# Optimization experiments

Hardware: AMD Instinct MI355X
Metric: run time of the kernel (lower is better)

The kernel has to match this reference:

```python
import jax, jax.numpy as jnp
import numpy as np

HEADS = 12
DIM_HEAD = 64

def setup_inputs() -> dict:
    key = jax.random.key(0)
    ks = jax.random.split(key, 5)
    B, S, D = 4, 2048, 768
    s = 0.02
    return {
        "x": jax.random.normal(ks[0], (B, S, D), dtype=jnp.float32),
        "Wq": jax.random.normal(ks[1], (D, D), dtype=jnp.float32) * s,
        "Wk": jax.random.normal(ks[2], (D, D), dtype=jnp.float32) * s,
        "Wv": jax.random.normal(ks[3], (D, D), dtype=jnp.float32) * s,
        "Wo": jax.random.normal(ks[4], (D, D), dtype=jnp.float32) * s,
        "bo": jnp.zeros((D,), dtype=jnp.float32),
    }

def reference(x, Wq, Wk, Wv, Wo, bo):
    B, S, D = x.shape
    H, Dh = HEADS, DIM_HEAD
    scale = Dh ** -0.5
    # projections (torch Linear: x @ W^T)
    q = (x @ Wq.T).reshape(B, S, H, Dh).transpose(0, 2, 1, 3) * scale  # [B,H,S,Dh]
    k = (x @ Wk.T).reshape(B, S, H, Dh).transpose(0, 2, 1, 3)
    v = (x @ Wv.T).reshape(B, S, H, Dh).transpose(0, 2, 1, 3)
    sim = jnp.einsum("bhid,bhjd->bhij", q, k)  # [B,H,S,S]
    mask_value = -jnp.finfo(sim.dtype).max
    causal_mask = jnp.triu(jnp.ones((S, S), dtype=bool), k=1)
    sim = jnp.where(causal_mask, mask_value, sim)
    attn = jax.nn.softmax(sim, axis=-1)
    # dropout is identity in eval mode
    out = jnp.einsum("bhij,bhjd->bhid", attn, v)  # [B,H,S,Dh]
    out = out.transpose(0, 2, 1, 3).reshape(B, S, H * Dh)
    return out @ Wo.T + bo
```

## Files before the change

kernel.cpp:

```cpp
#include <hip/hip_runtime.h>
#include <stdint.h>

typedef unsigned short u16;
typedef __bf16 bf16x8 __attribute__((ext_vector_type(8)));
typedef float f32x4 __attribute__((ext_vector_type(4)));
typedef u16 u16x4 __attribute__((ext_vector_type(4)));
typedef u16 u16x8 __attribute__((ext_vector_type(8)));
typedef uint32_t u32x2 __attribute__((ext_vector_type(2)));

#define LDS_CAST(p) (reinterpret_cast<__attribute__((address_space(3))) uint32_t*>(reinterpret_cast<uintptr_t>(p)))
#define GLB_CAST(p) (reinterpret_cast<const __attribute__((address_space(1))) uint32_t*>(reinterpret_cast<uintptr_t>(p)))
#define GLOAD16(g, l) __builtin_amdgcn_global_load_lds(GLB_CAST(g), LDS_CAST(l), 16, 0, 0)
#define AS3U16(p) (reinterpret_cast<__attribute__((address_space(3))) u16*>(reinterpret_cast<uintptr_t>(p)))

__device__ __forceinline__ u16 f2bf(float f) {
    uint32_t u = __builtin_bit_cast(uint32_t, f);
    u += 0x7fffu + ((u >> 16) & 1u);
    return (u16)(u >> 16);
}
__device__ __forceinline__ u16 bfbits(float f) {
    return __builtin_bit_cast(u16, (__bf16)f);
}

__global__ void cast_all(const float* __restrict__ x,
                         const float* __restrict__ a, const float* __restrict__ b,
                         const float* __restrict__ c, const float* __restrict__ d,
                         u16* __restrict__ ox, u16* __restrict__ oa, u16* __restrict__ ob,
                         u16* __restrict__ oc, u16* __restrict__ od) {
    const int bid = blockIdx.x;
    const float* in;
    u16* out;
    int i;
    if (bid < 6144) {
        in = x; out = ox; i = bid * 256 + threadIdx.x;
    } else {
        const int zb = bid - 6144;
        const int z = zb / 576, lb = zb % 576;
        in = (z == 0) ? a : (z == 1) ? b : (z == 2) ? c : d;
        out = (z == 0) ? oa : (z == 1) ? ob : (z == 2) ? oc : od;
        i = lb * 256 + threadIdx.x;
    }
    float4 f = reinterpret_cast<const float4*>(in)[i];
    u16x4 o;
    o.x = f2bf(f.x); o.y = f2bf(f.y); o.z = f2bf(f.z); o.w = f2bf(f.w);
    reinterpret_cast<u16x4*>(out)[i] = o;
}

__global__ __launch_bounds__(256) void gemm_qkv(
    const u16* __restrict__ X, const u16* __restrict__ Wq,
    const u16* __restrict__ Wk, const u16* __restrict__ Wv,
    u16* __restrict__ qo, u16* __restrict__ ko, u16* __restrict__ vTo)
{
    __shared__ u16 As[2][128 * 32];
    __shared__ u16 Bs[2][128 * 32];
    const int tid = threadIdx.x;
    const int lane = tid & 63;
    const int w = tid >> 6;
    const int lr = lane & 15, lg = lane >> 4;
    const int wrow = (w >> 1) * 64, wcol = (w & 1) * 64;

    const int lin = blockIdx.x + blockIdx.y * 6 + blockIdx.z * 384;
    const int xcd = lin & 7, idx = lin >> 3;
    const int prow = xcd * 8 + idx / 18;
    const int rem = idx % 18;
    const int bxc = rem % 6, z = rem / 6;
    const int row0 = prow * 128, col0 = bxc * 128;
    const u16* Wt = (z == 0) ? Wq : (z == 1) ? Wk : Wv;

    f32x4 acc[4][4];
#pragma unroll
    for (int m = 0; m < 4; ++m)
#pragma unroll
        for (int n = 0; n < 4; ++n)
#pragma unroll
            for (int j = 0; j < 4; ++j) acc[m][n][j] = 0.f;

#define QSTAGE(KT)                                                                                 \
    {                                                                                              \
        const int buf_ = (KT) & 1;                                                                 \
        _Pragma("unroll")                                                                          \
        for (int it = 0; it < 2; ++it) {                                                           \
            const int c = it * 256 + w * 64 + lane;                                                \
            const int row = c >> 2, c16 = c & 3;                                                   \
            GLOAD16(X  + (size_t)(row0 + row) * 768 + (KT) * 32 + c16 * 8, &As[buf_][(it * 256 + w * 64) * 8]); \
            GLOAD16(Wt + (size_t)(col0 + row) * 768 + (KT) * 32 + c16 * 8, &Bs[buf_][(it * 256 + w * 64) * 8]); \
        }                                                                                          \
    }

#define QSTEP(KT, VN, PF)                                                                          \
    {                                                                                              \
        if (PF) QSTAGE((KT) + 1);                                                                  \
        asm volatile("s_waitcnt vmcnt(" #VN ")" ::: "memory");                                     \
        __builtin_amdgcn_s_barrier();                                                              \
        const int cur_ = (KT) & 1;                                                                 \
        bf16x8 af[4], bfr[4];                                                                      \
        _Pragma("unroll")                                                                          \
        for (int m = 0; m < 4; ++m) af[m] = *(const bf16x8*)&As[cur_][(wrow + m * 16 + lr) * 32 + lg * 8]; \
        _Pragma("unroll")                                                                          \
        for (int n = 0; n < 4; ++n) bfr[n] = *(const bf16x8*)&Bs[cur_][(wcol + n * 16 + lr) * 32 + lg * 8]; \
        asm volatile("s_waitcnt lgkmcnt(0)" ::: "memory");                                         \
        __builtin_amdgcn_sched_barrier(0);                                                         \
        __builtin_amdgcn_s_barrier();                                                              \
        _Pragma("unroll")                                                                          \
        for (int m = 0; m < 4; ++m)                                                                \
            _Pragma("unroll")                                                                      \
            for (int n = 0; n < 4; ++n)                                                            \
                acc[m][n] = __builtin_amdgcn_mfma_f32_16x16x32_bf16(af[m], bfr[n], acc[m][n], 0, 0, 0); \
    }

    QSTAGE(0);
    for (int kt = 0; kt < 23; ++kt) QSTEP(kt, 4, true);
    QSTEP(23, 0, false);
#undef QSTEP
#undef QSTAGE

    if (z == 2) {
#pragma unroll
        for (int n = 0; n < 4; ++n) {
            const int j = col0 + wcol + n * 16 + lr;
            const int h = j >> 6, dh = j & 63;
#pragma unroll
            for (int m = 0; m < 4; ++m) {
                const int i0 = row0 + wrow + m * 16 + lg * 4;
                const int b = i0 >> 11, s0 = i0 & 2047;
                u16x4 pk;
#pragma unroll
                for (int r = 0; r < 4; ++r) pk[r] = bfbits(acc[m][n][r]);
                *(u16x4*)&vTo[(((size_t)b * 12 + h) * 64 + dh) * 2048 + s0] = pk;
            }
        }
    } else {
        u16* outp = (z == 0) ? qo : ko;
        const float scl = (z == 0) ? 0.18033688011112042f : 1.0f;
#pragma unroll
        for (int n = 0; n < 4; ++n) {
            const int j = col0 + wcol + n * 16 + lr;
            const int h = j >> 6, dh = j & 63;
#pragma unroll
            for (int m = 0; m < 4; ++m)
#pragma unroll
                for (int r = 0; r < 4; ++r) {
                    const int i = row0 + wrow + m * 16 + lg * 4 + r;
                    const int b = i >> 11, s = i & 2047;
                    outp[(((size_t)b * 12 + h) * 2048 + s) * 64 + dh] = bfbits(acc[m][n][r] * scl);
                }
        }
    }
}

template<bool DIAG>
__device__ __forceinline__ void attn_step(
    const bf16x8* aq, f32x4* o, float* lrow,
    const u16* __restrict__ Ksb, const u16* __restrict__ Vsb, u16* __restrict__ PT,
    int kvb, int qg0, int lr, int lg)
{
    f32x4 sacc[4];
#pragma unroll
    for (int n = 0; n < 4; ++n)
#pragma unroll
        for (int j = 0; j < 4; ++j) sacc[n][j] = 0.f;
    __builtin_amdgcn_s_setprio(1);
#pragma unroll
    for (int kk = 0; kk < 2; ++kk)
#pragma unroll
        for (int n = 0; n < 4; ++n) {
            const int row = n * 16 + lr;
            const int p = (kk * 4 + lg) ^ (row & 7);
            bf16x8 bk = *(const bf16x8*)&Ksb[row * 64 + p * 8];
            sacc[n] = __builtin_amdgcn_mfma_f32_16x16x32_bf16(aq[kk], bk, sacc[n], 0, 0, 0);
        }
    __builtin_amdgcn_s_setprio(0);

    float pv[4][4];
#pragma unroll
    for (int r = 0; r < 4; ++r) {
        float ls = 0.f;
#pragma unroll
        for (int n = 0; n < 4; ++n) {
            float sv = sacc[n][r];
            if (DIAG && (kvb + n * 16 + lr) > qg0 + r) sv = -1e30f;
            const float e = __builtin_amdgcn_exp2f(sv);
            pv[r][n] = e;
            ls += e;
        }
        lrow[r] += ls;
    }

#pragma unroll
    for (int n = 0; n < 4; ++n) {
        u16x4 pk;
#pragma unroll
        for (int r = 0; r < 4; ++r) pk[r] = bfbits(pv[r][n]);
        *(u16x4*)&PT[(n * 16 + lr) * 16 + lg * 4] = pk;
    }

    u32x2 t0, t1, t2, t3;
    __attribute__((address_space(3))) u16* pb = AS3U16(PT) + lg * 128 + lr * 4;
    asm volatile("ds_read_b64_tr_b16 %0, %1" : "=v"(t0) : "v"(pb) : "memory");
    asm volatile("ds_read_b64_tr_b16 %0, %1 offset:128" : "=v"(t1) : "v"(pb) : "memory");
    asm volatile("ds_read_b64_tr_b16 %0, %1 offset:1024" : "=v"(t2) : "v"(pb) : "memory");
    asm volatile("ds_read_b64_tr_b16 %0, %1 offset:1152" : "=v"(t3) : "v"(pb) : "memory");
    asm volatile("s_waitcnt lgkmcnt(0)" ::: "memory");
    __builtin_amdgcn_sched_barrier(0);
    union { u32x2 h[2]; bf16x8 v; } ua, ub;
    ua.h[0] = t0; ua.h[1] = t1;
    ub.h[0] = t2; ub.h[1] = t3;
    const bf16x8 ap0 = ua.v, ap1 = ub.v;

    __builtin_amdgcn_s_setprio(1);
#pragma unroll
    for (int n = 0; n < 4; ++n) {
        const int rowv = n * 16 + lr;
        const int p0 = (0 + lg) ^ (rowv & 7);
        const int p1 = (4 + lg) ^ (rowv & 7);
        bf16x8 bv0 = *(const bf16x8*)&Vsb[rowv * 64 + p0 * 8];
        bf16x8 bv1 = *(const bf16x8*)&Vsb[rowv * 64 + p1 * 8];
        o[n] = __builtin_amdgcn_mfma_f32_16x16x32_bf16(ap0, bv0, o[n], 0, 0, 0);
        o[n] = __builtin_amdgcn_mfma_f32_16x16x32_bf16(ap1, bv1, o[n], 0, 0, 0);
    }
    __builtin_amdgcn_s_setprio(0);
}

__global__ __launch_bounds__(256) void attn_kernel(
    const u16* __restrict__ q, const u16* __restrict__ k,
    const u16* __restrict__ vT, u16* __restrict__ attn)
{
    __shared__ u16 Ks[2][64 * 64];
    __shared__ u16 Vs[2][64 * 64];
    __shared__ u16 Ps[4][64 * 16];

    const int lin = blockIdx.x + (blockIdx.y << 4);
    const int logi = (lin & 7) * 96 + (lin >> 3);
    const int pair = logi & 15, bh = logi >> 4;

    const int qA = pair, qB = 31 - pair;
    const int tid = threadIdx.x, lane = tid & 63, w = tid >> 6;
    const int lr = lane & 15, lg = lane >> 4;

    const u16* Kp = k + (size_t)bh * 2048 * 64;
    const u16* Vp = vT + (size_t)bh * 64 * 2048;

    const u16* QpA = q + ((size_t)bh * 2048 + qA * 64 + w * 16) * 64;
    const u16* QpB = q + ((size_t)bh * 2048 + qB * 64 + w * 16) * 64;
    bf16x8 aqA[2], aqB[2];
    aqA[0] = *(const bf16x8*)&QpA[lr * 64 + lg * 8];
    aqA[1] = *(const bf16x8*)&QpA[lr * 64 + 32 + lg * 8];
    aqB[0] = *(const bf16x8*)&QpB[lr * 64 + lg * 8];
    aqB[1] = *(const bf16x8*)&QpB[lr * 64 + 32 + lg * 8];

    f32x4 oA[4], oB[4];
    float lA[4], lB[4];
#pragma unroll
    for (int n = 0; n < 4; ++n)
#pragma unroll
        for (int j = 0; j < 4; ++j) { oA[n][j] = 0.f; oB[n][j] = 0.f; }
#pragma unroll
    for (int r = 0; r < 4; ++r) { lA[r] = 0.f; lB[r] = 0.f; }

#define STAGE(T, BUF)                                                                        \
    {                                                                                        \
        _Pragma("unroll")                                                                    \
        for (int it = 0; it < 2; ++it) {                                                     \
            const int c = it * 256 + w * 64 + lane;                                          \
            const int row = c >> 3, pc = c & 7;                                              \
            const int lc = pc ^ (row & 7);                                                   \
            GLOAD16(Kp + (size_t)((T) * 64 + row) * 64 + lc * 8, &Ks[BUF][(it * 256 + w * 64) * 8]); \
            GLOAD16(Vp + (size_t)row * 2048 + (T) * 64 + lc * 8, &Vs[BUF][(it * 256 + w * 64) * 8]); \
        }                                                                                    \
    }

    STAGE(0, 0);
    const int qg0A = qA * 64 + w * 16 + lg * 4;
    const int qg0B = qB * 64 + w * 16 + lg * 4;

    int t = 0;
    for (; t < qA; ++t) {
        const int cur = t & 1;
        __syncthreads();
        STAGE(t + 1, cur ^ 1);
        attn_step<false>(aqB, oB, lB, Ks[cur], Vs[cur], Ps[w], t * 64, qg0B, lr, lg);
        attn_step<false>(aqA, oA, lA, Ks[cur], Vs[cur], Ps[w], t * 64, qg0A, lr, lg);
    }
    {
        const int cur = t & 1;
        __syncthreads();
        STAGE(t + 1, cur ^ 1);
        attn_step<false>(aqB, oB, lB, Ks[cur], Vs[cur], Ps[w], t * 64, qg0B, lr, lg);
        attn_step<true >(aqA, oA, lA, Ks[cur], Vs[cur], Ps[w], t * 64, qg0A, lr, lg);
        ++t;
    }
    for (; t < qB; ++t) {
        const int cur = t & 1;
        __syncthreads();
        STAGE(t + 1, cur ^ 1);
        attn_step<false>(aqB, oB, lB, Ks[cur], Vs[cur], Ps[w], t * 64, qg0B, lr, lg);
    }
    {
        const int cur = t & 1;
        __syncthreads();
        attn_step<true >(aqB, oB, lB, Ks[cur], Vs[cur], Ps[w], t * 64, qg0B, lr, lg);
    }
#undef STAGE

#pragma unroll
    for (int r = 0; r < 4; ++r) {
#pragma unroll
        for (int off = 1; off < 16; off <<= 1) {
            lA[r] += __shfl_xor(lA[r], off);
            lB[r] += __shfl_xor(lB[r], off);
        }
        lA[r] = 1.f / lA[r];
        lB[r] = 1.f / lB[r];
    }

    const int b = bh / 12, h = bh - b * 12;
#pragma unroll
    for (int n = 0; n < 4; ++n)
#pragma unroll
        for (int r = 0; r < 4; ++r) {
            const int sA = qA * 64 + w * 16 + lg * 4 + r;
            const int sB = qB * 64 + w * 16 + lg * 4 + r;
            attn[((size_t)b * 2048 + sA) * 768 + h * 64 + n * 16 + lr] = bfbits(oA[n][r] * lA[r]);
            attn[((size_t)b * 2048 + sB) * 768 + h * 64 + n * 16 + lr] = bfbits(oB[n][r] * lB[r]);
        }
}

__global__ __launch_bounds__(256) void gemm_out(
    const u16* __restrict__ A, const u16* __restrict__ Wo,
    const float* __restrict__ bo, float* __restrict__ out)
{
    __shared__ u16 As[2][64 * 32];
    __shared__ u16 Bs[2][128 * 32];
    const int tid = threadIdx.x;
    const int lane = tid & 63;
    const int w = tid >> 6;
    const int lr = lane & 15, lg = lane >> 4;
    const int wrow = (w >> 1) * 32, wcol = (w & 1) * 64;

    const int lin = blockIdx.x + blockIdx.y * 6;
    const int xcd = lin & 7, idx = lin >> 3;
    const int prow = xcd * 16 + idx / 6;
    const int bxc = idx % 6;
    const int row0 = prow * 64, col0 = bxc * 128;

    f32x4 acc[2][4];
#pragma unroll
    for (int m = 0; m < 2; ++m)
#pragma unroll
        for (int n = 0; n < 4; ++n)
#pragma unroll
            for (int j = 0; j < 4; ++j) acc[m][n][j] = 0.f;

#define OSTAGE(KT)                                                                                 \
    {                                                                                              \
        const int buf_ = (KT) & 1;                                                                 \
        {                                                           \
            const int c = w * 64 + lane;                                                           \
            const int row = c >> 2, c16 = c & 3;                                                   \
            GLOAD16(A + (size_t)(row0 + row) * 768 + (KT) * 32 + c16 * 8, &As[buf_][c * 8]);       \
        }                                                                                          \
        _Pragma("unroll")                                                                          \
        for (int it = 0; it < 2; ++it) {                          \
            const int c = it * 256 + w * 64 + lane;                                                \
            const int row = c >> 2, c16 = c & 3;                                                   \
            GLOAD16(Wo + (size_t)(col0 + row) * 768 + (KT) * 32 + c16 * 8, &Bs[buf_][c * 8]);      \
        }                                                                                          \
    }

#define OSTEP(KT, VN, PF)                                                                          \
    {                                                                                              \
        if (PF) OSTAGE((KT) + 1);                                                                  \
        asm volatile("s_waitcnt vmcnt(" #VN ")" ::: "memory");                                     \
        __builtin_amdgcn_s_barrier();                                                              \
        const int cur_ = (KT) & 1;                                                                 \
        bf16x8 af[2], bfr[4];                                                                      \
        _Pragma("unroll")                                                                          \
        for (int m = 0; m < 2; ++m) af[m] = *(const bf16x8*)&As[cur_][(wrow + m * 16 + lr) * 32 + lg * 8]; \
        _Pragma("unroll")                                                                          \
        for (int n = 0; n < 4; ++n) bfr[n] = *(const bf16x8*)&Bs[cur_][(wcol + n * 16 + lr) * 32 + lg * 8]; \
        asm volatile("s_waitcnt lgkmcnt(0)" ::: "memory");                                         \
        __builtin_amdgcn_sched_barrier(0);                                                         \
        __builtin_amdgcn_s_barrier();                                                              \
        _Pragma("unroll")                                                                          \
        for (int m = 0; m < 2; ++m)                                                                \
            _Pragma("unroll")                                                                      \
            for (int n = 0; n < 4; ++n)                                                            \
                acc[m][n] = __builtin_amdgcn_mfma_f32_16x16x32_bf16(af[m], bfr[n], acc[m][n], 0, 0, 0); \
    }

    OSTAGE(0);
    for (int kt = 0; kt < 23; ++kt) OSTEP(kt, 3, true);
    OSTEP(23, 0, false);
#undef OSTEP
#undef OSTAGE

#pragma unroll
    for (int n = 0; n < 4; ++n) {
        const int j = col0 + wcol + n * 16 + lr;
        const float bj = bo[j];
#pragma unroll
        for (int m = 0; m < 2; ++m)
#pragma unroll
            for (int r = 0; r < 4; ++r) {
                const int i = row0 + wrow + m * 16 + lg * 4 + r;
                out[(size_t)i * 768 + j] = acc[m][n][r] + bj;
            }
    }
}

extern "C" void kernel_launch(void* const* d_in, const int* in_sizes, int n_in,
                              void* d_out, int out_size, void* d_ws, size_t ws_size,
                              hipStream_t stream) {
    const float* x  = (const float*)d_in[0];
    const float* Wq = (const float*)d_in[1];
    const float* Wk = (const float*)d_in[2];
    const float* Wv = (const float*)d_in[3];
    const float* Wo = (const float*)d_in[4];
    const float* bo = (const float*)d_in[5];
    float* out = (float*)d_out;

    const size_t NX = 6291456;
    const size_t NW = 589824;
    if (ws_size < (NX * 4 + NW * 4 + NX) * sizeof(u16)) return;
    u16* ws  = (u16*)d_ws;
    u16* xb  = ws;
    u16* wqb = xb  + NX;
    u16* wkb = wqb + NW;
    u16* wvb = wkb + NW;
    u16* wob = wvb + NW;
    u16* qb_ = wob + NW;
    u16* kb_ = qb_ + NX;
    u16* vtb = kb_ + NX;
    u16* ab_ = vtb + NX;

    cast_all<<<6144 + 2304, 256, 0, stream>>>(x, Wq, Wk, Wv, Wo, xb, wqb, wkb, wvb, wob);

    gemm_qkv<<<dim3(6, 64, 3), 256, 0, stream>>>(xb, wqb, wkb, wvb, qb_, kb_, vtb);
    attn_kernel<<<dim3(16, 48), 256, 0, stream>>>(qb_, kb_, vtb, ab_);
    gemm_out<<<dim3(6, 128), 256, 0, stream>>>(ab_, wob, bo, out);
}
```

Baseline: 126.6 us.

## Fuse fp32-to-bf16 conversion of x into QKV GEMM A-tile staging

Drops the separate cast pass over the activation tensor x. The QKV GEMM now reads fp32 x directly into registers, converts to bf16, and writes the A tile into LDS after the MFMAs of each step, while the weights still use async global-to-LDS loads. This removes a full read and write of x and the bf16 workspace copy. In exchange, each GEMM block reads twice as many A bytes (fp32) many times over through the caches, and the A path goes through registers with an extra lgkmcnt wait.

```diff
diff --git a/kernel.cpp b/kernel.cpp
--- a/kernel.cpp
+++ b/kernel.cpp
@@ -22,24 +22,14 @@
     return __builtin_bit_cast(u16, (__bf16)f);
 }
 
-__global__ void cast_all(const float* __restrict__ x,
-                         const float* __restrict__ a, const float* __restrict__ b,
-                         const float* __restrict__ c, const float* __restrict__ d,
-                         u16* __restrict__ ox, u16* __restrict__ oa, u16* __restrict__ ob,
-                         u16* __restrict__ oc, u16* __restrict__ od) {
-    const int bid = blockIdx.x;
-    const float* in;
-    u16* out;
-    int i;
-    if (bid < 6144) {
-        in = x; out = ox; i = bid * 256 + threadIdx.x;
-    } else {
-        const int zb = bid - 6144;
-        const int z = zb / 576, lb = zb % 576;
-        in = (z == 0) ? a : (z == 1) ? b : (z == 2) ? c : d;
-        out = (z == 0) ? oa : (z == 1) ? ob : (z == 2) ? oc : od;
-        i = lb * 256 + threadIdx.x;
-    }
+__global__ void cast_w(const float* __restrict__ a, const float* __restrict__ b,
+                       const float* __restrict__ c, const float* __restrict__ d,
+                       u16* __restrict__ oa, u16* __restrict__ ob,
+                       u16* __restrict__ oc, u16* __restrict__ od) {
+    const int z = blockIdx.x / 576, lb = blockIdx.x % 576;
+    const float* in = (z == 0) ? a : (z == 1) ? b : (z == 2) ? c : d;
+    u16* out = (z == 0) ? oa : (z == 1) ? ob : (z == 2) ? oc : od;
+    const int i = lb * 256 + threadIdx.x;
     float4 f = reinterpret_cast<const float4*>(in)[i];
     u16x4 o;
     o.x = f2bf(f.x); o.y = f2bf(f.y); o.z = f2bf(f.z); o.w = f2bf(f.w);
@@ -47,7 +37,7 @@
 }
 
 __global__ __launch_bounds__(256) void gemm_qkv(
-    const u16* __restrict__ X, const u16* __restrict__ Wq,
+    const float* __restrict__ Xf, const u16* __restrict__ Wq,
     const u16* __restrict__ Wk, const u16* __restrict__ Wv,
     u16* __restrict__ qo, u16* __restrict__ ko, u16* __restrict__ vTo)
 {
@@ -67,6 +57,11 @@
     const int row0 = prow * 128, col0 = bxc * 128;
     const u16* Wt = (z == 0) ? Wq : (z == 1) ? Wk : Wv;
 
+    const int arow = tid >> 1, acol = (tid & 1) * 16;
+    const float* Xbase = Xf + (size_t)(row0 + arow) * 768 + acol;
+    u16* Adst0 = &As[0][arow * 32 + acol];
+    u16* Adst1 = &As[1][arow * 32 + acol];
+
     f32x4 acc[4][4];
 #pragma unroll
     for (int m = 0; m < 4; ++m)
@@ -75,22 +70,42 @@
 #pragma unroll
             for (int j = 0; j < 4; ++j) acc[m][n][j] = 0.f;
 
-#define QSTAGE(KT)                                                                                 \
+    float4 fa0, fa1, fa2, fa3;
+#define QLOAD_A(KT)                                                                                \
+    {                                                                                              \
+        const float* s_ = Xbase + (KT) * 32;                                                       \
+        fa0 = *(const float4*)(s_);                                                                \
+        fa1 = *(const float4*)(s_ + 4);                                                            \
+        fa2 = *(const float4*)(s_ + 8);                                                            \
+        fa3 = *(const float4*)(s_ + 12);                                                           \
+    }
+#define QWRITE_A(KT)                                                                               \
+    {                                                                                              \
+        u16x8 p0, p1;                                                                              \
+        p0[0] = bfbits(fa0.x); p0[1] = bfbits(fa0.y); p0[2] = bfbits(fa0.z); p0[3] = bfbits(fa0.w);\
+        p0[4] = bfbits(fa1.x); p0[5] = bfbits(fa1.y); p0[6] = bfbits(fa1.z); p0[7] = bfbits(fa1.w);\
+        p1[0] = bfbits(fa2.x); p1[1] = bfbits(fa2.y); p1[2] = bfbits(fa2.z); p1[3] = bfbits(fa2.w);\
+        p1[4] = bfbits(fa3.x); p1[5] = bfbits(fa3.y); p1[6] = bfbits(fa3.z); p1[7] = bfbits(fa3.w);\
+        u16* d_ = ((KT) & 1) ? Adst1 : Adst0;                                                      \
+        *(u16x8*)d_ = p0;                                                                          \
+        *(u16x8*)(d_ + 8) = p1;                                                                    \
+    }
+#define QSTAGE_W(KT)                                                                               \
     {                                                                                              \
         const int buf_ = (KT) & 1;                                                                 \
         _Pragma("unroll")                                                                          \
         for (int it = 0; it < 2; ++it) {                                                           \
             const int c = it * 256 + w * 64 + lane;                                                \
             const int row = c >> 2, c16 = c & 3;                                                   \
-            GLOAD16(X  + (size_t)(row0 + row) * 768 + (KT) * 32 + c16 * 8, &As[buf_][(it * 256 + w * 64) * 8]); \
             GLOAD16(Wt + (size_t)(col0 + row) * 768 + (KT) * 32 + c16 * 8, &Bs[buf_][(it * 256 + w * 64) * 8]); \
         }                                                                                          \
     }
 
 #define QSTEP(KT, VN, PF)                                                                          \
     {                                                                                              \
-        if (PF) QSTAGE((KT) + 1);                                                                  \
+        if (PF) { QLOAD_A((KT) + 1); QSTAGE_W((KT) + 1); }                                         \
         asm volatile("s_waitcnt vmcnt(" #VN ")" ::: "memory");                                     \
+        asm volatile("s_waitcnt lgkmcnt(0)" ::: "memory");                                         \
         __builtin_amdgcn_s_barrier();                                                              \
         const int cur_ = (KT) & 1;                                                                 \
         bf16x8 af[4], bfr[4];                                                                      \
@@ -106,13 +121,16 @@
             _Pragma("unroll")                                                                      \
             for (int n = 0; n < 4; ++n)                                                            \
                 acc[m][n] = __builtin_amdgcn_mfma_f32_16x16x32_bf16(af[m], bfr[n], acc[m][n], 0, 0, 0); \
-    }
-
-    QSTAGE(0);
-    for (int kt = 0; kt < 23; ++kt) QSTEP(kt, 4, true);
+        if (PF) QWRITE_A((KT) + 1);                                                                \
+    }
+
+    QLOAD_A(0); QSTAGE_W(0); QWRITE_A(0);
+    for (int kt = 0; kt < 23; ++kt) QSTEP(kt, 6, true);
     QSTEP(23, 0, false);
 #undef QSTEP
-#undef QSTAGE
+#undef QSTAGE_W
+#undef QWRITE_A
+#undef QLOAD_A
 
     if (z == 2) {
 #pragma unroll
@@ -421,10 +439,9 @@
 
     const size_t NX = 6291456;
     const size_t NW = 589824;
-    if (ws_size < (NX * 4 + NW * 4 + NX) * sizeof(u16)) return;
+    if (ws_size < (NX * 4 + NW * 4) * sizeof(u16)) return;
     u16* ws  = (u16*)d_ws;
-    u16* xb  = ws;
-    u16* wqb = xb  + NX;
+    u16* wqb = ws;
     u16* wkb = wqb + NW;
     u16* wvb = wkb + NW;
     u16* wob = wvb + NW;
@@ -433,9 +450,9 @@
     u16* vtb = kb_ + NX;
     u16* ab_ = vtb + NX;
 
-    cast_all<<<6144 + 2304, 256, 0, stream>>>(x, Wq, Wk, Wv, Wo, xb, wqb, wkb, wvb, wob);
-
-    gemm_qkv<<<dim3(6, 64, 3), 256, 0, stream>>>(xb, wqb, wkb, wvb, qb_, kb_, vtb);
+    cast_w<<<2304, 256, 0, stream>>>(Wq, Wk, Wv, Wo, wqb, wkb, wvb, wob);
+
+    gemm_qkv<<<dim3(6, 64, 3), 256, 0, stream>>>(x, wqb, wkb, wvb, qb_, kb_, vtb);
     attn_kernel<<<dim3(16, 48), 256, 0, stream>>>(qb_, kb_, vtb, ab_);
     gemm_out<<<dim3(6, 128), 256, 0, stream>>>(ab_, wob, bo, out);
 }
```

After: 158.1 us. 1.25x slower.

## Compute Q, K and V in one block sharing the X tile

Applied to the files above, without the earlier changes.

The QKV projection kernel now has each block compute all three outputs (Q, K, V) for one 128x128 tile. The X tile is loaded once and reused across the three weight matrices, instead of three blocks each reloading it. This cuts the grid from 1152 to 384 blocks and triples the accumulator registers (192 floats per thread), raising register pressure and LDS use. The MFMAs are also moved before the LDS barrier, so with fewer blocks per CU occupancy and latency hiding may suffer.

```diff
diff --git a/kernel.cpp b/kernel.cpp
--- a/kernel.cpp
+++ b/kernel.cpp
@@ -46,34 +46,34 @@
     reinterpret_cast<u16x4*>(out)[i] = o;
 }
 
-__global__ __launch_bounds__(256) void gemm_qkv(
+__global__ __launch_bounds__(256, 2) void gemm_qkv(
     const u16* __restrict__ X, const u16* __restrict__ Wq,
     const u16* __restrict__ Wk, const u16* __restrict__ Wv,
     u16* __restrict__ qo, u16* __restrict__ ko, u16* __restrict__ vTo)
 {
     __shared__ u16 As[2][128 * 32];
-    __shared__ u16 Bs[2][128 * 32];
+    __shared__ u16 Bs[3][2][128 * 32];
     const int tid = threadIdx.x;
     const int lane = tid & 63;
     const int w = tid >> 6;
     const int lr = lane & 15, lg = lane >> 4;
     const int wrow = (w >> 1) * 64, wcol = (w & 1) * 64;
 
-    const int lin = blockIdx.x + blockIdx.y * 6 + blockIdx.z * 384;
+    const int lin = blockIdx.x + blockIdx.y * 6;
     const int xcd = lin & 7, idx = lin >> 3;
-    const int prow = xcd * 8 + idx / 18;
-    const int rem = idx % 18;
-    const int bxc = rem % 6, z = rem / 6;
+    const int prow = xcd * 8 + idx / 6;
+    const int bxc = idx % 6;
     const int row0 = prow * 128, col0 = bxc * 128;
-    const u16* Wt = (z == 0) ? Wq : (z == 1) ? Wk : Wv;
-
-    f32x4 acc[4][4];
-#pragma unroll
-    for (int m = 0; m < 4; ++m)
-#pragma unroll
-        for (int n = 0; n < 4; ++n)
-#pragma unroll
-            for (int j = 0; j < 4; ++j) acc[m][n][j] = 0.f;
+
+    f32x4 acc[3][4][4];
+#pragma unroll
+    for (int zz = 0; zz < 3; ++zz)
+#pragma unroll
+        for (int m = 0; m < 4; ++m)
+#pragma unroll
+            for (int n = 0; n < 4; ++n)
+#pragma unroll
+                for (int j = 0; j < 4; ++j) acc[zz][m][n][j] = 0.f;
 
 #define QSTAGE(KT)                                                                                 \
     {                                                                                              \
@@ -82,8 +82,12 @@
         for (int it = 0; it < 2; ++it) {                                                           \
             const int c = it * 256 + w * 64 + lane;                                                \
             const int row = c >> 2, c16 = c & 3;                                                   \
-            GLOAD16(X  + (size_t)(row0 + row) * 768 + (KT) * 32 + c16 * 8, &As[buf_][(it * 256 + w * 64) * 8]); \
-            GLOAD16(Wt + (size_t)(col0 + row) * 768 + (KT) * 32 + c16 * 8, &Bs[buf_][(it * 256 + w * 64) * 8]); \
+            const size_t go = (size_t)row * 768 + (KT) * 32 + c16 * 8;                             \
+            const int lo = (it * 256 + w * 64) * 8;                                                \
+            GLOAD16(X  + (size_t)row0 * 768 + go, &As[buf_][lo]);                                  \
+            GLOAD16(Wq + (size_t)col0 * 768 + go, &Bs[0][buf_][lo]);                               \
+            GLOAD16(Wk + (size_t)col0 * 768 + go, &Bs[1][buf_][lo]);                               \
+            GLOAD16(Wv + (size_t)col0 * 768 + go, &Bs[2][buf_][lo]);                               \
         }                                                                                          \
     }
 
@@ -93,28 +97,50 @@
         asm volatile("s_waitcnt vmcnt(" #VN ")" ::: "memory");                                     \
         __builtin_amdgcn_s_barrier();                                                              \
         const int cur_ = (KT) & 1;                                                                 \
-        bf16x8 af[4], bfr[4];                                                                      \
+        bf16x8 af[4];                                                                              \
         _Pragma("unroll")                                                                          \
         for (int m = 0; m < 4; ++m) af[m] = *(const bf16x8*)&As[cur_][(wrow + m * 16 + lr) * 32 + lg * 8]; \
         _Pragma("unroll")                                                                          \
-        for (int n = 0; n < 4; ++n) bfr[n] = *(const bf16x8*)&Bs[cur_][(wcol + n * 16 + lr) * 32 + lg * 8]; \
+        for (int zz = 0; zz < 3; ++zz) {                                                           \
+            bf16x8 bfr[4];                                                                         \
+            _Pragma("unroll")                                                                      \
+            for (int n = 0; n < 4; ++n) bfr[n] = *(const bf16x8*)&Bs[zz][cur_][(wcol + n * 16 + lr) * 32 + lg * 8]; \
+            _Pragma("unroll")                                                                      \
+            for (int m = 0; m < 4; ++m)                                                            \
+                _Pragma("unroll")                                                                  \
+                for (int n = 0; n < 4; ++n)                                                        \
+                    acc[zz][m][n] = __builtin_amdgcn_mfma_f32_16x16x32_bf16(af[m], bfr[n], acc[zz][m][n], 0, 0, 0); \
+        }                                                                                          \
         asm volatile("s_waitcnt lgkmcnt(0)" ::: "memory");                                         \
         __builtin_amdgcn_sched_barrier(0);                                                         \
         __builtin_amdgcn_s_barrier();                                                              \
-        _Pragma("unroll")                                                                          \
-        for (int m = 0; m < 4; ++m)                                                                \
-            _Pragma("unroll")                                                                      \
-            for (int n = 0; n < 4; ++n)                                                            \
-                acc[m][n] = __builtin_amdgcn_mfma_f32_16x16x32_bf16(af[m], bfr[n], acc[m][n], 0, 0, 0); \
     }
 
     QSTAGE(0);
-    for (int kt = 0; kt < 23; ++kt) QSTEP(kt, 4, true);
+    for (int kt = 0; kt < 23; ++kt) QSTEP(kt, 8, true);
     QSTEP(23, 0, false);
 #undef QSTEP
 #undef QSTAGE
 
-    if (z == 2) {
+#pragma unroll
+    for (int zz = 0; zz < 2; ++zz) {
+        u16* outp = (zz == 0) ? qo : ko;
+        const float scl = (zz == 0) ? 0.18033688011112042f : 1.0f;
+#pragma unroll
+        for (int n = 0; n < 4; ++n) {
+            const int j = col0 + wcol + n * 16 + lr;
+            const int h = j >> 6, dh = j & 63;
+#pragma unroll
+            for (int m = 0; m < 4; ++m)
+#pragma unroll
+                for (int r = 0; r < 4; ++r) {
+                    const int i = row0 + wrow + m * 16 + lg * 4 + r;
+                    const int b = i >> 11, s = i & 2047;
+                    outp[(((size_t)b * 12 + h) * 2048 + s) * 64 + dh] = bfbits(acc[zz][m][n][r] * scl);
+                }
+        }
+    }
+    {
 #pragma unroll
         for (int n = 0; n < 4; ++n) {
             const int j = col0 + wcol + n * 16 + lr;
@@ -125,25 +151,9 @@
                 const int b = i0 >> 11, s0 = i0 & 2047;
                 u16x4 pk;
 #pragma unroll
-                for (int r = 0; r < 4; ++r) pk[r] = bfbits(acc[m][n][r]);
+                for (int r = 0; r < 4; ++r) pk[r] = bfbits(acc[2][m][n][r]);
                 *(u16x4*)&vTo[(((size_t)b * 12 + h) * 64 + dh) * 2048 + s0] = pk;
             }
-        }
-    } else {
-        u16* outp = (z == 0) ? qo : ko;
-        const float scl = (z == 0) ? 0.18033688011112042f : 1.0f;
-#pragma unroll
-        for (int n = 0; n < 4; ++n) {
-            const int j = col0 + wcol + n * 16 + lr;
-            const int h = j >> 6, dh = j & 63;
-#pragma unroll
-            for (int m = 0; m < 4; ++m)
-#pragma unroll
-                for (int r = 0; r < 4; ++r) {
-                    const int i = row0 + wrow + m * 16 + lg * 4 + r;
-                    const int b = i >> 11, s = i & 2047;
-                    outp[(((size_t)b * 12 + h) * 2048 + s) * 64 + dh] = bfbits(acc[m][n][r] * scl);
-                }
         }
     }
 }
@@ -435,7 +445,7 @@
 
     cast_all<<<6144 + 2304, 256, 0, stream>>>(x, Wq, Wk, Wv, Wo, xb, wqb, wkb, wvb, wob);
 
-    gemm_qkv<<<dim3(6, 64, 3), 256, 0, stream>>>(xb, wqb, wkb, wvb, qb_, kb_, vtb);
+    gemm_qkv<<<dim3(6, 64), 256, 0, stream>>>(xb, wqb, wkb, wvb, qb_, kb_, vtb);
     attn_kernel<<<dim3(16, 48), 256, 0, stream>>>(qb_, kb_, vtb, ab_);
     gemm_out<<<dim3(6, 128), 256, 0, stream>>>(ab_, wob, bo, out);
 }
```

After: 120.8 us, median of 2. 4.6% less time.
